# Kernel optimization log

Hardware: AMD Instinct MI355X
Metric: run time of the kernel (lower is better)

The kernel has to match this reference:

```python
import jax, jax.numpy as jnp
import numpy as np

INPUT_DIM = 1024
HIDDEN = 1024
MASKED = INPUT_DIM // 2  # even indices are the conditioning half
BATCH = 65536


def setup_inputs() -> dict:
    key = jax.random.key(0)
    ks = jax.random.split(key, 7)
    s1 = 1.0 / np.sqrt(MASKED)
    s2 = 1.0 / np.sqrt(HIDDEN)
    x = jax.random.normal(ks[0], (BATCH, INPUT_DIM), dtype=jnp.float32)
    W1 = jax.random.uniform(ks[1], (MASKED, HIDDEN), jnp.float32, -s1, s1)
    b1 = jax.random.uniform(ks[2], (HIDDEN,), jnp.float32, -s1, s1)
    W2 = jax.random.uniform(ks[3], (HIDDEN, HIDDEN), jnp.float32, -s2, s2)
    b2 = jax.random.uniform(ks[4], (HIDDEN,), jnp.float32, -s2, s2)
    W3 = jax.random.uniform(ks[5], (HIDDEN, INPUT_DIM - MASKED), jnp.float32, -s2, s2)
    b3 = jax.random.uniform(ks[6], (INPUT_DIM - MASKED,), jnp.float32, -s2, s2)
    return {"x": x, "W1": W1, "b1": b1, "W2": W2, "b2": b2, "W3": W3, "b3": b3}


def reference(x, W1, b1, W2, b2, W3, b3):
    # mask_type='even': mask[::2]=1 -> even indices conditioning, odd indices translated
    masked = x[:, 0::2]  # [B, MASKED], gather of conditioning half
    h = jax.nn.relu(masked @ W1 + b1)
    h = jax.nn.relu(h @ W2 + b2)
    translation = h @ W3 + b3  # [B, INPUT_DIM - MASKED]
    # scatter-add translation into odd positions
    y = x.at[:, 1::2].add(translation)
    return y
```

## Files before the change

### kernel.cpp

```cpp
#include <hip/hip_runtime.h>
#include <stdint.h>

#define BATCH  65536
#define IN_DIM 1024
#define MASKED 512
#define HIDDEN 1024

typedef unsigned short u16;
typedef __bf16 bf16x8 __attribute__((ext_vector_type(8)));
typedef float  f32x4  __attribute__((ext_vector_type(4)));

typedef __attribute__((address_space(1))) void gvoid;
typedef __attribute__((address_space(3))) void lvoid;

#define WAITV(N) asm volatile("s_waitcnt vmcnt(" #N ")" ::: "memory")
#define WAITL0() asm volatile("s_waitcnt lgkmcnt(0)" ::: "memory")
#define FENCE()  asm volatile("" ::: "memory")

__device__ __forceinline__ u16 f32_to_bf16(float f) {
    union { float f; uint32_t u; } v; v.f = f;
    uint32_t r = v.u + 0x7FFFu + ((v.u >> 16) & 1u);
    return (u16)(r >> 16);
}

__global__ void prep_xm(const float* __restrict__ x, u16* __restrict__ xm) {
    int idx = blockIdx.x * blockDim.x + threadIdx.x;
    const float4* xv = reinterpret_cast<const float4*>(x);
    float4 v0 = xv[idx * 2];
    float4 v1 = xv[idx * 2 + 1];
    ushort4 o;
    o.x = f32_to_bf16(v0.x);
    o.y = f32_to_bf16(v0.z);
    o.z = f32_to_bf16(v1.x);
    o.w = f32_to_bf16(v1.z);
    reinterpret_cast<ushort4*>(xm)[idx] = o;
}

__global__ void wconv(const float* __restrict__ W, u16* __restrict__ Wt,
                      int K, int N) {
    __shared__ float t[32][33];
    const int nbk = K / 32;
    const int bk = blockIdx.x % nbk;
    const int bn = blockIdx.x / nbk;
    const int tx = threadIdx.x & 31;
    const int ty = threadIdx.x >> 5;
    const int k0 = bk * 32, n0 = bn * 32;
    #pragma unroll
    for (int i = 0; i < 4; ++i)
        t[ty + i * 8][tx] = W[(int64_t)(k0 + ty + i * 8) * N + n0 + tx];
    __syncthreads();
    #pragma unroll
    for (int i = 0; i < 4; ++i)
        Wt[(int64_t)(n0 + ty + i * 8) * K + k0 + tx] = f32_to_bf16(t[tx][ty + i * 8]);
}

template<int K, int N, int MODE>
__global__ __launch_bounds__(512, 2)
void gemm256(const u16* __restrict__ A, const u16* __restrict__ Bt,
             const float* __restrict__ bias,
             u16* __restrict__ Cb,
             const float* __restrict__ X,
             float* __restrict__ Y) {
    constexpr int BK = 32;
    constexpr int NT = K / BK;
    __shared__ __align__(16) u16 As[4][256 * BK];
    __shared__ __align__(16) u16 Bs[4][256 * BK];

    const int tid  = threadIdx.x;
    const int lane = tid & 63;
    const int w    = tid >> 6;
    const int wm   = w >> 2;
    const int wn   = w & 3;

    const int nwg = gridDim.x;
    const int cpx = nwg >> 3;
    const int bid = (blockIdx.x & 7) * cpx + (blockIdx.x >> 3);
    constexpr int nbn = N / 256;
    const int m0 = (bid / nbn) * 256;
    const int n0 = (bid % nbn) * 256;

    const int srow = w * 16 + (lane >> 2);
    const int sg   = ((lane & 3) ^ ((lane >> 3) & 3)) * 8;
    const u16* aS = A  + (int64_t)(m0 + srow) * K + sg;
    const u16* bS = Bt + (int64_t)(n0 + srow) * K + sg;
    const int lOff = w * 512;

#define STG_A1(kt) __builtin_amdgcn_global_load_lds((gvoid*)(aS + (kt)*BK),          (lvoid*)(&As[(kt)&3][lOff]),        16, 0, 0)
#define STG_A2(kt) __builtin_amdgcn_global_load_lds((gvoid*)(aS + 128*K + (kt)*BK),  (lvoid*)(&As[(kt)&3][4096 + lOff]), 16, 0, 0)
#define STG_B1(kt) __builtin_amdgcn_global_load_lds((gvoid*)(bS + (kt)*BK),          (lvoid*)(&Bs[(kt)&3][lOff]),        16, 0, 0)
#define STG_B2(kt) __builtin_amdgcn_global_load_lds((gvoid*)(bS + 128*K + (kt)*BK),  (lvoid*)(&Bs[(kt)&3][4096 + lOff]), 16, 0, 0)

    f32x4 acc[8][4];
    #pragma unroll
    for (int i = 0; i < 8; ++i)
        #pragma unroll
        for (int j = 0; j < 4; ++j)
            acc[i][j] = f32x4{0.f, 0.f, 0.f, 0.f};

    STG_A1(0); STG_A2(0); STG_B1(0); STG_B2(0);
    STG_A1(1); STG_A2(1); STG_B1(1); STG_B2(1);
    STG_A1(2); STG_A2(2); STG_B1(2); STG_B2(2);
    WAITV(8);
    __builtin_amdgcn_s_barrier();
    FENCE();

    const int arow = wm * 128 + (lane & 15);
    const int brow = wn * 64  + (lane & 15);
    const int kcol = ((lane >> 4) ^ (((lane & 15) >> 1) & 3)) * 8;

    for (int kt = 0; kt < NT; ++kt) {
        const int s = kt & 3;
        const u16* Asl = As[s];
        const u16* Bsl = Bs[s];
        bf16x8 a[4], b[4];

        #pragma unroll
        for (int mf = 0; mf < 4; ++mf)
            a[mf] = *reinterpret_cast<const bf16x8*>(&Asl[(arow + mf * 16) * BK + kcol]);
        #pragma unroll
        for (int nf = 0; nf < 4; ++nf)
            b[nf] = *reinterpret_cast<const bf16x8*>(&Bsl[(brow + nf * 16) * BK + kcol]);
        if (kt + 3 < NT) { STG_A1(kt + 3); STG_B1(kt + 3); }
        __builtin_amdgcn_s_setprio(1);
        #pragma unroll
        for (int mf = 0; mf < 4; ++mf)
            #pragma unroll
            for (int nf = 0; nf < 4; ++nf)
                acc[mf][nf] = __builtin_amdgcn_mfma_f32_16x16x32_bf16(
                    a[mf], b[nf], acc[mf][nf], 0, 0, 0);
        __builtin_amdgcn_s_setprio(0);
        __builtin_amdgcn_s_barrier();
        FENCE();

        bf16x8 a2[4];
        #pragma unroll
        for (int mf = 0; mf < 4; ++mf)
            a2[mf] = *reinterpret_cast<const bf16x8*>(&Asl[(arow + 64 + mf * 16) * BK + kcol]);
        if (kt + 3 < NT) { STG_A2(kt + 3); STG_B2(kt + 3); }
        __builtin_amdgcn_s_setprio(1);
        #pragma unroll
        for (int mf = 0; mf < 4; ++mf)
            #pragma unroll
            for (int nf = 0; nf < 4; ++nf)
                acc[mf + 4][nf] = __builtin_amdgcn_mfma_f32_16x16x32_bf16(
                    a2[mf], b[nf], acc[mf + 4][nf], 0, 0, 0);
        __builtin_amdgcn_s_setprio(0);

        WAITL0();
        __builtin_amdgcn_sched_barrier(0);
        if (kt < NT - 3)       { WAITV(8); }
        else if (kt == NT - 3) { WAITV(4); }
        else if (kt == NT - 2) { WAITV(0); }
        if (kt < NT - 1) {
            __builtin_amdgcn_s_barrier();
            FENCE();
        }
    }

    const int cl = lane & 15;
    const int rg = (lane >> 4) * 4;
    #pragma unroll
    for (int nf = 0; nf < 4; ++nf) {
        const int n  = n0 + wn * 64 + nf * 16 + cl;
        const float bv = bias[n];
        #pragma unroll
        for (int mf = 0; mf < 8; ++mf) {
            #pragma unroll
            for (int r = 0; r < 4; ++r) {
                const int m = m0 + wm * 128 + mf * 16 + rg + r;
                float v = acc[mf][nf][r] + bv;
                if (MODE == 0) {
                    v = v > 0.f ? v : 0.f;
                    Cb[(int64_t)m * N + n] = f32_to_bf16(v);
                } else {
                    const int64_t p = (int64_t)m * IN_DIM + 2 * n;
                    float2 xv = *reinterpret_cast<const float2*>(&X[p]);
                    float2 o;
                    o.x = xv.x;
                    o.y = xv.y + v;
                    *reinterpret_cast<float2*>(&Y[p]) = o;
                }
            }
        }
    }
#undef STG_A1
#undef STG_A2
#undef STG_B1
#undef STG_B2
}

extern "C" void kernel_launch(void* const* d_in, const int* in_sizes, int n_in,
                              void* d_out, int out_size, void* d_ws, size_t ws_size,
                              hipStream_t stream) {
    const float* x  = (const float*)d_in[0];
    const float* W1 = (const float*)d_in[1];
    const float* b1 = (const float*)d_in[2];
    const float* W2 = (const float*)d_in[3];
    const float* b2 = (const float*)d_in[4];
    const float* W3 = (const float*)d_in[5];
    const float* b3 = (const float*)d_in[6];
    float* y = (float*)d_out;

    char* ws = (char*)d_ws;
    u16* h1  = (u16*)(ws);
    u16* h2  = (u16*)(ws + 134217728);
    u16* xm  = (u16*)(ws + 134217728);
    u16* W1t = (u16*)(ws + 268435456);
    u16* W2t = (u16*)(ws + 268435456 + 1048576);
    u16* W3t = (u16*)(ws + 268435456 + 1048576 + 2097152);

    prep_xm<<<BATCH * IN_DIM / 8 / 256, 256, 0, stream>>>(x, xm);

    wconv<<<(MASKED / 32) * (HIDDEN / 32), 256, 0, stream>>>(W1, W1t, MASKED, HIDDEN);
    wconv<<<(HIDDEN / 32) * (HIDDEN / 32), 256, 0, stream>>>(W2, W2t, HIDDEN, HIDDEN);
    wconv<<<(HIDDEN / 32) * ((IN_DIM - MASKED) / 32), 256, 0, stream>>>(W3, W3t, HIDDEN, IN_DIM - MASKED);

    gemm256<MASKED, HIDDEN, 0><<<(BATCH / 256) * (HIDDEN / 256), 512, 0, stream>>>(
        xm, W1t, b1, h1, nullptr, nullptr);
    gemm256<HIDDEN, HIDDEN, 0><<<(BATCH / 256) * (HIDDEN / 256), 512, 0, stream>>>(
        h1, W2t, b2, h2, nullptr, nullptr);
    gemm256<HIDDEN, IN_DIM - MASKED, 1><<<(BATCH / 256) * ((IN_DIM - MASKED) / 256), 512, 0, stream>>>(
        h2, W3t, b3, nullptr, x, y);
}
```

Before: 521.4 us.

## Restructure GEMM mainloop into 8-phase ping-pong pipeline with BK=64 stages

Replaces the 4-stage BK=32 LDS ring with a double-buffered BK=64 layout split into k-halves, using four MFMA phases per iteration. Each phase issues a finer-grained global-to-LDS load of a quarter tile, and the explicit lgkmcnt wait is dropped. The aim is to interleave loads with MFMA work more evenly and cut the number of barriers per unit of K work. The cost is a more intricate wait-count scheme, where a miscount could cause races or stalls, and the same 128KB of LDS in use.

```diff
diff --git a/kernel.cpp b/kernel.cpp
--- a/kernel.cpp
+++ b/kernel.cpp
@@ -14,7 +14,6 @@
 typedef __attribute__((address_space(3))) void lvoid;
 
 #define WAITV(N) asm volatile("s_waitcnt vmcnt(" #N ")" ::: "memory")
-#define WAITL0() asm volatile("s_waitcnt lgkmcnt(0)" ::: "memory")
 #define FENCE()  asm volatile("" ::: "memory")
 
 __device__ __forceinline__ u16 f32_to_bf16(float f) {
@@ -56,15 +55,13 @@
 
 template<int K, int N, int MODE>
 __global__ __launch_bounds__(512, 2)
-void gemm256(const u16* __restrict__ A, const u16* __restrict__ Bt,
-             const float* __restrict__ bias,
-             u16* __restrict__ Cb,
-             const float* __restrict__ X,
-             float* __restrict__ Y) {
-    constexpr int BK = 32;
-    constexpr int NT = K / BK;
-    __shared__ __align__(16) u16 As[4][256 * BK];
-    __shared__ __align__(16) u16 Bs[4][256 * BK];
+void gemm8p(const u16* __restrict__ A, const u16* __restrict__ Bt,
+            const float* __restrict__ bias,
+            u16* __restrict__ Cb,
+            const float* __restrict__ X,
+            float* __restrict__ Y) {
+    constexpr int NT = K / 64;
+    __shared__ __align__(16) u16 Ls[65536];
 
     const int tid  = threadIdx.x;
     const int lane = tid & 63;
@@ -79,16 +76,20 @@
     const int m0 = (bid / nbn) * 256;
     const int n0 = (bid % nbn) * 256;
 
-    const int srow = w * 16 + (lane >> 2);
-    const int sg   = ((lane & 3) ^ ((lane >> 3) & 3)) * 8;
-    const u16* aS = A  + (int64_t)(m0 + srow) * K + sg;
-    const u16* bS = Bt + (int64_t)(n0 + srow) * K + sg;
-    const int lOff = w * 512;
-
-#define STG_A1(kt) __builtin_amdgcn_global_load_lds((gvoid*)(aS + (kt)*BK),          (lvoid*)(&As[(kt)&3][lOff]),        16, 0, 0)
-#define STG_A2(kt) __builtin_amdgcn_global_load_lds((gvoid*)(aS + 128*K + (kt)*BK),  (lvoid*)(&As[(kt)&3][4096 + lOff]), 16, 0, 0)
-#define STG_B1(kt) __builtin_amdgcn_global_load_lds((gvoid*)(bS + (kt)*BK),          (lvoid*)(&Bs[(kt)&3][lOff]),        16, 0, 0)
-#define STG_B2(kt) __builtin_amdgcn_global_load_lds((gvoid*)(bS + 128*K + (kt)*BK),  (lvoid*)(&Bs[(kt)&3][4096 + lOff]), 16, 0, 0)
+    const u16* aPanel = A  + (int64_t)m0 * K;
+    const u16* bPanel = Bt + (int64_t)n0 * K;
+
+    auto stage = [&](int arrBase, int pp, int kh, const u16* gbase, int koff) {
+        #pragma unroll
+        for (int i = 0; i < 2; ++i) {
+            const int c = i * 512 + tid;
+            const int row = c >> 2;
+            const int cq = (c & 3) ^ ((row >> 1) & 3);
+            __builtin_amdgcn_global_load_lds(
+                (gvoid*)(gbase + (int64_t)row * K + koff + cq * 8),
+                (lvoid*)(&Ls[arrBase + pp * 16384 + kh * 8192 + c * 8]), 16, 0, 0);
+        }
+    };
 
     f32x4 acc[8][4];
     #pragma unroll
@@ -97,30 +98,35 @@
         for (int j = 0; j < 4; ++j)
             acc[i][j] = f32x4{0.f, 0.f, 0.f, 0.f};
 
-    STG_A1(0); STG_A2(0); STG_B1(0); STG_B2(0);
-    STG_A1(1); STG_A2(1); STG_B1(1); STG_B2(1);
-    STG_A1(2); STG_A2(2); STG_B1(2); STG_B2(2);
+    stage(0,     0, 0, aPanel, 0);
+    stage(0,     0, 1, aPanel, 32);
+    stage(32768, 0, 0, bPanel, 0);
+    stage(32768, 0, 1, bPanel, 32);
+    stage(0,     1, 0, aPanel, 64);
+    stage(32768, 1, 0, bPanel, 64);
+    stage(0,     1, 1, aPanel, 96);
+    stage(32768, 1, 1, bPanel, 96);
     WAITV(8);
-    __builtin_amdgcn_s_barrier();
-    FENCE();
-
-    const int arow = wm * 128 + (lane & 15);
-    const int brow = wn * 64  + (lane & 15);
-    const int kcol = ((lane >> 4) ^ (((lane & 15) >> 1) & 3)) * 8;
-
-    for (int kt = 0; kt < NT; ++kt) {
-        const int s = kt & 3;
-        const u16* Asl = As[s];
-        const u16* Bsl = Bs[s];
+    __builtin_amdgcn_s_barrier(); FENCE();
+
+    const int cl  = lane & 15;
+    const int rc  = (((lane >> 4) ^ ((cl >> 1) & 3))) * 8;
+    const int aR0 = (wm * 128 + cl) * 32;
+    const int bR0 = (wn * 64 + cl) * 32;
+
+    for (int t = 0; t < NT; ++t) {
+        const int p = t & 1;
+        const int ab = p * 16384;
+        const int bb = 32768 + p * 16384;
         bf16x8 a[4], b[4];
 
         #pragma unroll
         for (int mf = 0; mf < 4; ++mf)
-            a[mf] = *reinterpret_cast<const bf16x8*>(&Asl[(arow + mf * 16) * BK + kcol]);
+            a[mf] = *(const bf16x8*)&Ls[ab + aR0 + mf * 512 + rc];
         #pragma unroll
         for (int nf = 0; nf < 4; ++nf)
-            b[nf] = *reinterpret_cast<const bf16x8*>(&Bsl[(brow + nf * 16) * BK + kcol]);
-        if (kt + 3 < NT) { STG_A1(kt + 3); STG_B1(kt + 3); }
+            b[nf] = *(const bf16x8*)&Ls[bb + bR0 + nf * 512 + rc];
+        if (t >= 1 && t + 1 < NT) stage(0, (t + 1) & 1, 1, aPanel, (t + 1) * 64 + 32);
         __builtin_amdgcn_s_setprio(1);
         #pragma unroll
         for (int mf = 0; mf < 4; ++mf)
@@ -129,35 +135,56 @@
                 acc[mf][nf] = __builtin_amdgcn_mfma_f32_16x16x32_bf16(
                     a[mf], b[nf], acc[mf][nf], 0, 0, 0);
         __builtin_amdgcn_s_setprio(0);
-        __builtin_amdgcn_s_barrier();
-        FENCE();
-
-        bf16x8 a2[4];
-        #pragma unroll
-        for (int mf = 0; mf < 4; ++mf)
-            a2[mf] = *reinterpret_cast<const bf16x8*>(&Asl[(arow + 64 + mf * 16) * BK + kcol]);
-        if (kt + 3 < NT) { STG_A2(kt + 3); STG_B2(kt + 3); }
+        __builtin_amdgcn_s_barrier(); FENCE();
+
+        #pragma unroll
+        for (int mf = 0; mf < 4; ++mf)
+            a[mf] = *(const bf16x8*)&Ls[ab + aR0 + 64 * 32 + mf * 512 + rc];
+        if (t + 2 < NT) stage(32768, p, 0, bPanel, (t + 2) * 64);
         __builtin_amdgcn_s_setprio(1);
         #pragma unroll
         for (int mf = 0; mf < 4; ++mf)
             #pragma unroll
             for (int nf = 0; nf < 4; ++nf)
                 acc[mf + 4][nf] = __builtin_amdgcn_mfma_f32_16x16x32_bf16(
-                    a2[mf], b[nf], acc[mf + 4][nf], 0, 0, 0);
-        __builtin_amdgcn_s_setprio(0);
-
-        WAITL0();
-        __builtin_amdgcn_sched_barrier(0);
-        if (kt < NT - 3)       { WAITV(8); }
-        else if (kt == NT - 3) { WAITV(4); }
-        else if (kt == NT - 2) { WAITV(0); }
-        if (kt < NT - 1) {
-            __builtin_amdgcn_s_barrier();
-            FENCE();
-        }
+                    a[mf], b[nf], acc[mf + 4][nf], 0, 0, 0);
+        __builtin_amdgcn_s_setprio(0);
+        if (t + 2 < NT) { WAITV(10); } else { WAITV(0); }
+        __builtin_amdgcn_s_barrier(); FENCE();
+
+        #pragma unroll
+        for (int mf = 0; mf < 4; ++mf)
+            a[mf] = *(const bf16x8*)&Ls[ab + 8192 + aR0 + mf * 512 + rc];
+        #pragma unroll
+        for (int nf = 0; nf < 4; ++nf)
+            b[nf] = *(const bf16x8*)&Ls[bb + 8192 + bR0 + nf * 512 + rc];
+        if (t + 2 < NT) stage(0, p, 0, aPanel, (t + 2) * 64);
+        __builtin_amdgcn_s_setprio(1);
+        #pragma unroll
+        for (int mf = 0; mf < 4; ++mf)
+            #pragma unroll
+            for (int nf = 0; nf < 4; ++nf)
+                acc[mf][nf] = __builtin_amdgcn_mfma_f32_16x16x32_bf16(
+                    a[mf], b[nf], acc[mf][nf], 0, 0, 0);
+        __builtin_amdgcn_s_setprio(0);
+        __builtin_amdgcn_s_barrier(); FENCE();
+
+        #pragma unroll
+        for (int mf = 0; mf < 4; ++mf)
+            a[mf] = *(const bf16x8*)&Ls[ab + 8192 + aR0 + 64 * 32 + mf * 512 + rc];
+        if (t + 2 < NT) stage(32768, p, 1, bPanel, (t + 2) * 64 + 32);
+        __builtin_amdgcn_s_setprio(1);
+        #pragma unroll
+        for (int mf = 0; mf < 4; ++mf)
+            #pragma unroll
+            for (int nf = 0; nf < 4; ++nf)
+                acc[mf + 4][nf] = __builtin_amdgcn_mfma_f32_16x16x32_bf16(
+                    a[mf], b[nf], acc[mf + 4][nf], 0, 0, 0);
+        __builtin_amdgcn_s_setprio(0);
+        if (t + 2 < NT) { WAITV(10); } else { WAITV(0); }
+        __builtin_amdgcn_s_barrier(); FENCE();
     }
 
-    const int cl = lane & 15;
     const int rg = (lane >> 4) * 4;
     #pragma unroll
     for (int nf = 0; nf < 4; ++nf) {
@@ -173,20 +200,16 @@
                     v = v > 0.f ? v : 0.f;
                     Cb[(int64_t)m * N + n] = f32_to_bf16(v);
                 } else {
-                    const int64_t p = (int64_t)m * IN_DIM + 2 * n;
-                    float2 xv = *reinterpret_cast<const float2*>(&X[p]);
+                    const int64_t pp = (int64_t)m * IN_DIM + 2 * n;
+                    float2 xv = *reinterpret_cast<const float2*>(&X[pp]);
                     float2 o;
                     o.x = xv.x;
                     o.y = xv.y + v;
-                    *reinterpret_cast<float2*>(&Y[p]) = o;
+                    *reinterpret_cast<float2*>(&Y[pp]) = o;
                 }
             }
         }
     }
-#undef STG_A1
-#undef STG_A2
-#undef STG_B1
-#undef STG_B2
 }
 
 extern "C" void kernel_launch(void* const* d_in, const int* in_sizes, int n_in,
@@ -215,10 +238,10 @@
     wconv<<<(HIDDEN / 32) * (HIDDEN / 32), 256, 0, stream>>>(W2, W2t, HIDDEN, HIDDEN);
     wconv<<<(HIDDEN / 32) * ((IN_DIM - MASKED) / 32), 256, 0, stream>>>(W3, W3t, HIDDEN, IN_DIM - MASKED);
 
-    gemm256<MASKED, HIDDEN, 0><<<(BATCH / 256) * (HIDDEN / 256), 512, 0, stream>>>(
+    gemm8p<MASKED, HIDDEN, 0><<<(BATCH / 256) * (HIDDEN / 256), 512, 0, stream>>>(
         xm, W1t, b1, h1, nullptr, nullptr);
-    gemm256<HIDDEN, HIDDEN, 0><<<(BATCH / 256) * (HIDDEN / 256), 512, 0, stream>>>(
+    gemm8p<HIDDEN, HIDDEN, 0><<<(BATCH / 256) * (HIDDEN / 256), 512, 0, stream>>>(
         h1, W2t, b2, h2, nullptr, nullptr);
-    gemm256<HIDDEN, IN_DIM - MASKED, 1><<<(BATCH / 256) * ((IN_DIM - MASKED) / 256), 512, 0, stream>>>(
+    gemm8p<HIDDEN, IN_DIM - MASKED, 1><<<(BATCH / 256) * ((IN_DIM - MASKED) / 256), 512, 0, stream>>>(
         h2, W3t, b3, nullptr, x, y);
 }
```

After: 479.2 us. 1.09x faster.
